# Performance work log

Hardware: AMD Instinct MI355X
Metric: run time of the kernel (lower is better)

Reference implementation:

```python
import jax, jax.numpy as jnp
import numpy as np

S = 64        # num_states
ODIM = 8      # padded neighbor-feature width
H = 256       # HIDDEN_DIM
A = 16        # num_actions
B = 16384     # batch (dtpt)
IDIM = S + ODIM
NEG_SLOPE = 0.01  # nn.LeakyReLU default
EPS = 1e-5        # nn.LayerNorm default


def setup_inputs() -> dict:
    key = jax.random.key(0)
    ks = jax.random.split(key, 8)
    x = jax.random.normal(ks[0], (B, S), jnp.float32)
    # per-state neighbor indices into x's feature dim, padded to ODIM with a mask
    o_idx = jax.random.randint(ks[1], (S, ODIM), 0, S)
    o_len = jax.random.randint(ks[2], (S,), 1, ODIM + 1)
    o_mask = jnp.arange(ODIM)[None, :] < o_len[:, None]  # [S, ODIM] bool

    def lin(k, fin, fout):
        bound = 1.0 / np.sqrt(fin)
        kw, kb = jax.random.split(k)
        W = jax.random.uniform(kw, (S, fin, fout), jnp.float32, -bound, bound)
        b = jax.random.uniform(kb, (S, fout), jnp.float32, -bound, bound)
        return W, b

    W1, b1 = lin(ks[3], IDIM, H)
    W2, b2 = lin(ks[4], H, H)
    Wp, bp = lin(ks[5], H, A)
    g1 = jnp.ones((S, H), jnp.float32); be1 = jnp.zeros((S, H), jnp.float32)
    g2 = jnp.ones((S, H), jnp.float32); be2 = jnp.zeros((S, H), jnp.float32)
    return dict(x=x, o_idx=o_idx, o_mask=o_mask, W1=W1, b1=b1, g1=g1, be1=be1,
                W2=W2, b2=b2, g2=g2, be2=be2, Wp=Wp, bp=bp)


def _layer_norm(h, g, b):
    # h: [B, S, H], per-state affine params g,b: [S, H]
    mu = jnp.mean(h, axis=-1, keepdims=True)
    var = jnp.mean((h - mu) ** 2, axis=-1, keepdims=True)
    return (h - mu) * jax.lax.rsqrt(var + EPS) * g[None] + b[None]


def reference(x, o_idx, o_mask, W1, b1, g1, be1, W2, b2, g2, be2, Wp, bp):
    # irregular gather: for each state s take x[:, o_nbr_index[s]], zero-pad to ODIM
    o = jnp.where(o_mask[None, :, :], x[:, o_idx], jnp.float32(0))  # [B, S, ODIM]
    one_hot = jnp.broadcast_to(jnp.eye(S, dtype=x.dtype)[None], (x.shape[0], S, S))
    inp = jnp.concatenate([one_hot, o], axis=-1)  # [B, S, IDIM]

    h = jnp.einsum('bsi,sih->bsh', inp, W1) + b1[None]
    h = _layer_norm(jax.nn.leaky_relu(h, NEG_SLOPE), g1, be1)
    h = jnp.einsum('bsh,shk->bsk', h, W2) + b2[None]
    h = _layer_norm(jax.nn.leaky_relu(h, NEG_SLOPE), g2, be2)
    pi_logit = jnp.einsum('bsh,sha->bsa', h, Wp) + bp[None]  # [B, S, A]
    lg_sm = jax.nn.log_softmax(pi_logit, axis=-1)
    return pi_logit, lg_sm
```

## Files before the change

kernel.cpp:

```cpp
#include <hip/hip_runtime.h>

#define LNEPS 1e-5f

typedef __attribute__((ext_vector_type(8)))  short          bf16x8;
typedef __attribute__((ext_vector_type(8)))  unsigned short u16x8;
typedef __attribute__((ext_vector_type(4)))  float          f32x4;
typedef __attribute__((ext_vector_type(16))) float          f32x16;
typedef __attribute__((ext_vector_type(4)))  unsigned int   u32x4;

#define MFMA32(a, b, c) __builtin_amdgcn_mfma_f32_32x32x16_bf16((a), (b), (c), 0, 0, 0)

#define WS_W2G  0
#define WS_A1   8388608
#define WS_WPG  8912896
#define WS_UC2  10027008
#define WS_MIDX 10092544

union U8 { bf16x8 v; unsigned u[4]; };

__device__ __forceinline__ unsigned short f2bf(float v) {
  union { float f; unsigned u; } a; a.f = v;
  unsigned r = a.u + 0x7fffu + ((a.u >> 16) & 1u);
  return (unsigned short)(r >> 16);
}
__device__ __forceinline__ unsigned cvtpk(float lo, float hi) {
  unsigned r;
  asm("v_cvt_pk_bf16_f32 %0, %1, %2" : "=v"(r) : "v"(lo), "v"(hi));
  return r;
}
__device__ __forceinline__ void plswap(unsigned w, unsigned& lo, unsigned& hi) {
  unsigned a = w, b = w;
  asm volatile("v_permlane32_swap_b32 %0, %1" : "+v"(a), "+v"(b));
  lo = a; hi = b;
}

__global__ void prep_midx_k(const int* __restrict__ oidx,
                            const unsigned* __restrict__ mask32,
                            int* __restrict__ midx) {
  __shared__ int fgt1, ffl;
  const int t = threadIdx.x;
  if (t == 0) { fgt1 = 0; ffl = 0; }
  __syncthreads();
  if (t < 128) {
    unsigned wv = mask32[t];
    if (wv == 0x3f800000u) atomicOr(&ffl, 1);
    else if (wv > 1u)      atomicOr(&fgt1, 1);
  }
  __syncthreads();
  const int mode = ffl ? 2 : (fgt1 ? 1 : 0);
  int mv;
  if (mode == 2)      mv = (((const float*)mask32)[t] != 0.0f) ? 1 : 0;
  else if (mode == 1) mv = (int)((const unsigned char*)mask32)[t];
  else                mv = ((const int*)mask32)[t];
  midx[t] = (mv != 0) ? oidx[t] : -1;
}

__global__ __launch_bounds__(256) void prep_w2g_k(
    const float* __restrict__ W2, const float* __restrict__ g1,
    unsigned short* __restrict__ w2g) {
  const int tid = blockIdx.x * 256 + threadIdx.x;
  const int l = tid & 63;
  const int t = (tid >> 6) & 15;
  const int i = (tid >> 10) & 7;
  const int s = tid >> 13;
  const int n = i * 32 + (l & 31);
  const int h = l >> 5;
  const float* w = W2 + (size_t)s * 65536;
  const float* g = g1 + s * 256;
  u16x8 v;
#pragma unroll
  for (int j = 0; j < 8; ++j) {
    const int k = t * 16 + h * 8 + j;
    v[j] = f2bf(w[k * 256 + n] * g[k]);
  }
  ((u16x8*)w2g)[tid] = v;
}

__global__ __launch_bounds__(256) void prep_uc2_k(
    const float* __restrict__ W2, const float* __restrict__ g1,
    const float* __restrict__ be1, const float* __restrict__ b2,
    unsigned* __restrict__ uc2) {
  const int tid = blockIdx.x * 256 + threadIdx.x;
  const int s = tid >> 8, n = tid & 255;
  const float* w = W2 + (size_t)s * 65536 + n;
  const float* g = g1 + s * 256;
  const float* be = be1 + s * 256;
  float u = 0.f, c = 0.f;
#pragma unroll 8
  for (int k = 0; k < 256; ++k) {
    const float wk = w[k * 256];
    u = fmaf(wk, g[k], u);
    c = fmaf(wk, be[k], c);
  }
  c += b2[tid];
  uc2[tid] = (unsigned)f2bf(u) | ((unsigned)f2bf(c) << 16);
}

__global__ __launch_bounds__(256) void prep_a1_k(
    const float* __restrict__ W1, const float* __restrict__ b1,
    unsigned short* __restrict__ a1b) {
  const int tid = blockIdx.x * 256 + threadIdx.x;
  const int l = tid & 63;
  const int i = (tid >> 6) & 7;
  const int s = tid >> 9;
  const int n = i * 32 + (l & 31);
  const float* w = W1 + (size_t)s * 72 * 256;
  u16x8 v;
#pragma unroll
  for (int j = 0; j < 8; ++j) v[j] = 0;
  if (l < 32) {
#pragma unroll
    for (int j = 0; j < 8; ++j) v[j] = f2bf(w[(64 + j) * 256 + n]);
  } else {
    v[0] = f2bf(w[s * 256 + n] + b1[s * 256 + n]);
  }
  ((u16x8*)a1b)[tid] = v;
}

__global__ __launch_bounds__(256) void prep_wpg_k(
    const float* __restrict__ Wp, const float* __restrict__ g2,
    const float* __restrict__ be2, const float* __restrict__ bp,
    unsigned short* __restrict__ wpg) {
  const int tid = blockIdx.x * 256 + threadIdx.x;
  const int l = tid & 63;
  const int r = tid >> 6;
  const int t = r % 17;
  const int s = r / 17;
  const int a = l & 31;
  const int h = l >> 5;
  u16x8 v;
#pragma unroll
  for (int j = 0; j < 8; ++j) v[j] = 0;
  if (t < 16) {
    if (a < 16) {
      const float* w = Wp + (size_t)s * 4096;
      const float* g = g2 + s * 256;
#pragma unroll
      for (int j = 0; j < 8; ++j) {
        const int k = t * 16 + h * 8 + j;
        v[j] = f2bf(w[k * 16 + a] * g[k]);
      }
    }
  } else if (h == 0 && a < 16) {
    const float* w = Wp + (size_t)s * 4096;
    float up = 0.f, cp = 0.f;
#pragma unroll 8
    for (int k = 0; k < 256; ++k) {
      const float wk = w[k * 16 + a];
      up = fmaf(wk, g2[s * 256 + k], up);
      cp = fmaf(wk, be2[s * 256 + k], cp);
    }
    cp += bp[s * 16 + a];
    v[0] = f2bf(up); v[1] = f2bf(cp);
  }
  ((u16x8*)wpg)[tid] = v;
}

__device__ __forceinline__ void pack_tile(const f32x16& a, const int h,
                                          unsigned* f0, unsigned* f1) {
  unsigned lo[8], hi[8];
#pragma unroll
  for (int m = 0; m < 8; ++m) {
    unsigned w = cvtpk(a[2 * m], a[2 * m + 1]);
    plswap(w, lo[m], hi[m]);
  }
  f0[0] = h ? lo[2] : lo[0];
  f0[1] = h ? lo[3] : lo[1];
  f0[2] = h ? hi[2] : hi[0];
  f0[3] = h ? hi[3] : hi[1];
  f1[0] = h ? lo[6] : lo[4];
  f1[1] = h ? lo[7] : lo[5];
  f1[2] = h ? hi[6] : hi[4];
  f1[3] = h ? hi[7] : hi[5];
}

__global__ __launch_bounds__(512, 2) void actor_main(
    const float* __restrict__ x, const int* __restrict__ midx,
    const unsigned short* __restrict__ w2g, const unsigned* __restrict__ uc2,
    const unsigned short* __restrict__ a1b, const unsigned short* __restrict__ wpg,
    float* __restrict__ out) {
  extern __shared__ char lds[];
  const int tid = threadIdx.x;
  const int wv = tid >> 6;
  const int l = tid & 63;
  const int bl = l & 31;
  const int h = l >> 5;
  const int s = blockIdx.x >> 2;
  const int rowstart = (blockIdx.x & 3) << 12;

  {
    const u32x4* src = (const u32x4*)(w2g + (size_t)s * 65536);
    u32x4* dst = (u32x4*)lds;
#pragma unroll
    for (int i = 0; i < 16; ++i) dst[i * 512 + tid] = src[i * 512 + tid];
  }

  unsigned aext[8];
#pragma unroll
  for (int i = 0; i < 8; ++i) {
    const unsigned t = uc2[(s * 8 + i) * 32 + bl];
    aext[i] = h ? 0u : t;
  }
  const int4 mi4 = ((const int4*)(midx + s * 8))[h];
  const bf16x8* A1 = ((const bf16x8*)a1b) + (size_t)(s * 8) * 64 + l;
  const bf16x8* A3 = ((const bf16x8*)wpg) + (size_t)(s * 17) * 64 + l;

  __syncthreads();

  for (int it = 0; it < 16; ++it) {
    const int row = rowstart + it * 256 + wv * 32 + bl;

    const float* xr = x + (size_t)row * 64;
    const float ga = mi4.x < 0 ? 0.f : xr[mi4.x];
    const float gb = mi4.y < 0 ? 0.f : xr[mi4.y];
    const float gc = mi4.z < 0 ? 0.f : xr[mi4.z];
    const float gd = mi4.w < 0 ? 0.f : xr[mi4.w];
    unsigned oa0, ob0, oa1, ob1;
    plswap(cvtpk(ga, gb), oa0, ob0);
    plswap(cvtpk(gc, gd), oa1, ob1);
    U8 B1;
    B1.u[0] = h ? 0x00003F80u : oa0;
    B1.u[1] = h ? 0u : oa1;
    B1.u[2] = h ? 0u : ob0;
    B1.u[3] = h ? 0u : ob1;
    f32x16 acc1[8];
#pragma unroll
    for (int i = 0; i < 8; ++i) {
      f32x16 z = {};
      acc1[i] = MFMA32(A1[i * 64], B1.v, z);
    }

    float s0 = 0.f, s1 = 0.f, q0 = 0.f, q1 = 0.f;
#pragma unroll
    for (int i = 0; i < 8; ++i)
#pragma unroll
      for (int r = 0; r < 16; ++r) {
        float v = acc1[i][r];
        v = fmaxf(v, 0.01f * v);
        acc1[i][r] = v;
        if (r & 1) { s1 += v; q1 = fmaf(v, v, q1); }
        else       { s0 += v; q0 = fmaf(v, v, q0); }
      }
    float sum = s0 + s1, ssq = q0 + q1;
    sum += __shfl_xor(sum, 32, 64);
    ssq += __shfl_xor(ssq, 32, 64);
    const float m1 = sum * 0.00390625f;
    const float var1 = fmaf(ssq, 0.00390625f, -m1 * m1) + LNEPS;
    const float rho1 = rsqrtf(var1);
    const float std1 = var1 * rho1;
    const unsigned be2w = cvtpk(-m1, std1);

    unsigned yf[16][4];
#pragma unroll
    for (int i = 0; i < 8; ++i) pack_tile(acc1[i], h, yf[2 * i], yf[2 * i + 1]);

    f32x16 acc2[8];
#pragma unroll
    for (int i = 0; i < 8; ++i) { f32x16 z = {}; acc2[i] = z; }
#pragma unroll
    for (int t = 0; t < 16; ++t) {
      U8 Bf;
      Bf.u[0] = yf[t][0]; Bf.u[1] = yf[t][1]; Bf.u[2] = yf[t][2]; Bf.u[3] = yf[t][3];
#pragma unroll
      for (int i = 0; i < 8; ++i) {
        const bf16x8 Af = *(const bf16x8*)(lds + (((i << 4) + t) << 10) + (l << 4));
        acc2[i] = MFMA32(Af, Bf.v, acc2[i]);
      }
    }
    {
      U8 Bx; Bx.u[0] = h ? 0u : be2w; Bx.u[1] = 0; Bx.u[2] = 0; Bx.u[3] = 0;
#pragma unroll
      for (int i = 0; i < 8; ++i) {
        U8 Ax; Ax.u[0] = aext[i]; Ax.u[1] = 0; Ax.u[2] = 0; Ax.u[3] = 0;
        acc2[i] = MFMA32(Ax.v, Bx.v, acc2[i]);
      }
    }

    s0 = s1 = q0 = q1 = 0.f;
#pragma unroll
    for (int i = 0; i < 8; ++i)
#pragma unroll
      for (int r = 0; r < 16; ++r) {
        float v = acc2[i][r];
        v = fmaxf(v, 0.01f * v);
        acc2[i][r] = v;
        if (r & 1) { s1 += v; q1 = fmaf(v, v, q1); }
        else       { s0 += v; q0 = fmaf(v, v, q0); }
      }
    float sum2 = s0 + s1, ssq2 = q0 + q1;
    sum2 += __shfl_xor(sum2, 32, 64);
    ssq2 += __shfl_xor(ssq2, 32, 64);
    const float mp = sum2 * 0.00390625f;
    const float qp = ssq2 * 0.00390625f;
    const float var2 = rho1 * rho1 * fmaf(-mp, mp, qp) + LNEPS;
    const float rho2 = rsqrtf(var2);
    const float sigma = rho1 * rho2;
    const float inv = var2 * rho2 * std1;
    const unsigned be3w = cvtpk(-mp, inv);

#pragma unroll
    for (int i = 0; i < 8; ++i) pack_tile(acc2[i], h, yf[2 * i], yf[2 * i + 1]);

    f32x16 a3a = {}, a3b = {};
#pragma unroll
    for (int t = 0; t < 16; t += 2) {
      U8 B0, Bq;
      B0.u[0] = yf[t][0]; B0.u[1] = yf[t][1]; B0.u[2] = yf[t][2]; B0.u[3] = yf[t][3];
      Bq.u[0] = yf[t + 1][0]; Bq.u[1] = yf[t + 1][1]; Bq.u[2] = yf[t + 1][2]; Bq.u[3] = yf[t + 1][3];
      a3a = MFMA32(A3[t * 64], B0.v, a3a);
      a3b = MFMA32(A3[(t + 1) * 64], Bq.v, a3b);
    }
    {
      U8 Bx; Bx.u[0] = h ? 0u : be3w; Bx.u[1] = 0; Bx.u[2] = 0; Bx.u[3] = 0;
      a3a = MFMA32(A3[16 * 64], Bx.v, a3a);
    }
    float lg[8];
#pragma unroll
    for (int r = 0; r < 8; ++r) lg[r] = sigma * (a3a[r] + a3b[r]);
    float mx = fmaxf(fmaxf(fmaxf(lg[0], lg[1]), fmaxf(lg[2], lg[3])),
                     fmaxf(fmaxf(lg[4], lg[5]), fmaxf(lg[6], lg[7])));
    mx = fmaxf(mx, __shfl_xor(mx, 32, 64));
    float es = 0.f;
#pragma unroll
    for (int r = 0; r < 8; ++r) es += __expf(lg[r] - mx);
    es += __shfl_xor(es, 32, 64);
    const float lse = mx + __logf(es);

    const size_t ob = (((size_t)row << 6) + s) * 16 + (h << 2);
    f32x4 v0 = {lg[0], lg[1], lg[2], lg[3]};
    f32x4 v1 = {lg[4], lg[5], lg[6], lg[7]};
    *(f32x4*)(out + ob) = v0;
    *(f32x4*)(out + ob + 8) = v1;
    f32x4 w0 = {lg[0] - lse, lg[1] - lse, lg[2] - lse, lg[3] - lse};
    f32x4 w1 = {lg[4] - lse, lg[5] - lse, lg[6] - lse, lg[7] - lse};
    *(f32x4*)(out + 16777216 + ob) = w0;
    *(f32x4*)(out + 16777216 + ob + 8) = w1;
  }
}

extern "C" void kernel_launch(void* const* d_in, const int* in_sizes, int n_in,
                              void* d_out, int out_size, void* d_ws, size_t ws_size,
                              hipStream_t stream) {
  const float* x    = (const float*)d_in[0];
  const int*   oidx = (const int*)d_in[1];
  const unsigned* omask = (const unsigned*)d_in[2];
  const float* W1 = (const float*)d_in[3];
  const float* b1 = (const float*)d_in[4];
  const float* g1 = (const float*)d_in[5];
  const float* be1 = (const float*)d_in[6];
  const float* W2 = (const float*)d_in[7];
  const float* b2 = (const float*)d_in[8];
  const float* g2 = (const float*)d_in[9];
  const float* be2 = (const float*)d_in[10];
  const float* Wp = (const float*)d_in[11];
  const float* bp = (const float*)d_in[12];
  float* out = (float*)d_out;

  char* ws = (char*)d_ws;
  unsigned short* wsW2G = (unsigned short*)(ws + WS_W2G);
  unsigned short* wsA1  = (unsigned short*)(ws + WS_A1);
  unsigned short* wsWPG = (unsigned short*)(ws + WS_WPG);
  unsigned*       wsUC2 = (unsigned*)(ws + WS_UC2);
  int*            wsMIDX = (int*)(ws + WS_MIDX);

  prep_midx_k<<<1, 512, 0, stream>>>(oidx, omask, wsMIDX);
  prep_w2g_k<<<2048, 256, 0, stream>>>(W2, g1, wsW2G);
  prep_uc2_k<<<64, 256, 0, stream>>>(W2, g1, be1, b2, wsUC2);
  prep_a1_k<<<128, 256, 0, stream>>>(W1, b1, wsA1);
  prep_wpg_k<<<272, 256, 0, stream>>>(Wp, g2, be2, bp, wsWPG);

  hipFuncSetAttribute((const void*)actor_main,
                      hipFuncAttributeMaxDynamicSharedMemorySize, 131072);
  actor_main<<<256, 512, 131072, stream>>>(
      x, wsMIDX, wsW2G, wsUC2, wsA1, wsWPG, out);
}
```

Before: 327.9 us.

## Prefetch next gather, interleave packing with MFMAs, simplify permlane packing

Rewrites pack_tile to use paired permlane32 swaps instead of duplicate swaps plus per-half selects, which cuts VALU work. Moves the x gather for the next iteration ahead of the current iteration's compute so global load latency overlaps the MFMA work. Packing of layer outputs is interleaved with the activation/statistics loop, and the third GEMM's MFMAs are issued per tile as each tile is packed. LDS weight fragments are loaded in batches ahead of the MFMA group, which is wrapped in s_setprio. The paired swap changes the data mapping, so numerical correctness relies on the new swap layout matching the old selects.

```diff
diff --git a/kernel.cpp b/kernel.cpp
--- a/kernel.cpp
+++ b/kernel.cpp
@@ -27,6 +27,9 @@
   unsigned r;
   asm("v_cvt_pk_bf16_f32 %0, %1, %2" : "=v"(r) : "v"(lo), "v"(hi));
   return r;
+}
+__device__ __forceinline__ void swap2(unsigned& a, unsigned& b) {
+  asm volatile("v_permlane32_swap_b32 %0, %1" : "+v"(a), "+v"(b));
 }
 __device__ __forceinline__ void plswap(unsigned w, unsigned& lo, unsigned& hi) {
   unsigned a = w, b = w;
@@ -156,22 +159,15 @@
   ((u16x8*)wpg)[tid] = v;
 }
 
-__device__ __forceinline__ void pack_tile(const f32x16& a, const int h,
+__device__ __forceinline__ void pack_tile(const f32x16& a,
                                           unsigned* f0, unsigned* f1) {
-  unsigned lo[8], hi[8];
-#pragma unroll
-  for (int m = 0; m < 8; ++m) {
-    unsigned w = cvtpk(a[2 * m], a[2 * m + 1]);
-    plswap(w, lo[m], hi[m]);
-  }
-  f0[0] = h ? lo[2] : lo[0];
-  f0[1] = h ? lo[3] : lo[1];
-  f0[2] = h ? hi[2] : hi[0];
-  f0[3] = h ? hi[3] : hi[1];
-  f1[0] = h ? lo[6] : lo[4];
-  f1[1] = h ? lo[7] : lo[5];
-  f1[2] = h ? hi[6] : hi[4];
-  f1[3] = h ? hi[7] : hi[5];
+  unsigned w0 = cvtpk(a[0], a[1]),   w1 = cvtpk(a[2], a[3]);
+  unsigned w2 = cvtpk(a[4], a[5]),   w3 = cvtpk(a[6], a[7]);
+  unsigned w4 = cvtpk(a[8], a[9]),   w5 = cvtpk(a[10], a[11]);
+  unsigned w6 = cvtpk(a[12], a[13]), w7 = cvtpk(a[14], a[15]);
+  swap2(w0, w2); swap2(w1, w3); swap2(w4, w6); swap2(w5, w7);
+  f0[0] = w0; f0[1] = w1; f0[2] = w2; f0[3] = w3;
+  f1[0] = w4; f1[1] = w5; f1[2] = w6; f1[3] = w7;
 }
 
 __global__ __launch_bounds__(512, 2) void actor_main(
@@ -205,16 +201,18 @@
   const bf16x8* A1 = ((const bf16x8*)a1b) + (size_t)(s * 8) * 64 + l;
   const bf16x8* A3 = ((const bf16x8*)wpg) + (size_t)(s * 17) * 64 + l;
 
+  const float* xbase = x + (size_t)(rowstart + wv * 32 + bl) * 64;
+
+  float ga = mi4.x < 0 ? 0.f : xbase[mi4.x];
+  float gb = mi4.y < 0 ? 0.f : xbase[mi4.y];
+  float gc = mi4.z < 0 ? 0.f : xbase[mi4.z];
+  float gd = mi4.w < 0 ? 0.f : xbase[mi4.w];
+
   __syncthreads();
 
   for (int it = 0; it < 16; ++it) {
     const int row = rowstart + it * 256 + wv * 32 + bl;
 
-    const float* xr = x + (size_t)row * 64;
-    const float ga = mi4.x < 0 ? 0.f : xr[mi4.x];
-    const float gb = mi4.y < 0 ? 0.f : xr[mi4.y];
-    const float gc = mi4.z < 0 ? 0.f : xr[mi4.z];
-    const float gd = mi4.w < 0 ? 0.f : xr[mi4.w];
     unsigned oa0, ob0, oa1, ob1;
     plswap(cvtpk(ga, gb), oa0, ob0);
     plswap(cvtpk(gc, gd), oa1, ob1);
@@ -223,6 +221,15 @@
     B1.u[1] = h ? 0u : oa1;
     B1.u[2] = h ? 0u : ob0;
     B1.u[3] = h ? 0u : ob1;
+
+    {
+      const float* xn = xbase + (size_t)(((it + 1) & 15) * 256) * 64;
+      ga = mi4.x < 0 ? 0.f : xn[mi4.x];
+      gb = mi4.y < 0 ? 0.f : xn[mi4.y];
+      gc = mi4.z < 0 ? 0.f : xn[mi4.z];
+      gd = mi4.w < 0 ? 0.f : xn[mi4.w];
+    }
+
     f32x16 acc1[8];
 #pragma unroll
     for (int i = 0; i < 8; ++i) {
@@ -231,8 +238,9 @@
     }
 
     float s0 = 0.f, s1 = 0.f, q0 = 0.f, q1 = 0.f;
-#pragma unroll
-    for (int i = 0; i < 8; ++i)
+    unsigned yf[16][4];
+#pragma unroll
+    for (int i = 0; i < 8; ++i) {
 #pragma unroll
       for (int r = 0; r < 16; ++r) {
         float v = acc1[i][r];
@@ -241,6 +249,8 @@
         if (r & 1) { s1 += v; q1 = fmaf(v, v, q1); }
         else       { s0 += v; q0 = fmaf(v, v, q0); }
       }
+      pack_tile(acc1[i], yf[2 * i], yf[2 * i + 1]);
+    }
     float sum = s0 + s1, ssq = q0 + q1;
     sum += __shfl_xor(sum, 32, 64);
     ssq += __shfl_xor(ssq, 32, 64);
@@ -250,10 +260,6 @@
     const float std1 = var1 * rho1;
     const unsigned be2w = cvtpk(-m1, std1);
 
-    unsigned yf[16][4];
-#pragma unroll
-    for (int i = 0; i < 8; ++i) pack_tile(acc1[i], h, yf[2 * i], yf[2 * i + 1]);
-
     f32x16 acc2[8];
 #pragma unroll
     for (int i = 0; i < 8; ++i) { f32x16 z = {}; acc2[i] = z; }
@@ -261,11 +267,14 @@
     for (int t = 0; t < 16; ++t) {
       U8 Bf;
       Bf.u[0] = yf[t][0]; Bf.u[1] = yf[t][1]; Bf.u[2] = yf[t][2]; Bf.u[3] = yf[t][3];
-#pragma unroll
-      for (int i = 0; i < 8; ++i) {
-        const bf16x8 Af = *(const bf16x8*)(lds + (((i << 4) + t) << 10) + (l << 4));
-        acc2[i] = MFMA32(Af, Bf.v, acc2[i]);
-      }
+      bf16x8 Af[8];
+#pragma unroll
+      for (int i = 0; i < 8; ++i)
+        Af[i] = *(const bf16x8*)(lds + (((i << 4) + t) << 10) + (l << 4));
+      __builtin_amdgcn_s_setprio(1);
+#pragma unroll
+      for (int i = 0; i < 8; ++i) acc2[i] = MFMA32(Af[i], Bf.v, acc2[i]);
+      __builtin_amdgcn_s_setprio(0);
     }
     {
       U8 Bx; Bx.u[0] = h ? 0u : be2w; Bx.u[1] = 0; Bx.u[2] = 0; Bx.u[3] = 0;
@@ -276,9 +285,10 @@
       }
     }
 
+    f32x16 a3a = {}, a3b = {};
     s0 = s1 = q0 = q1 = 0.f;
 #pragma unroll
-    for (int i = 0; i < 8; ++i)
+    for (int i = 0; i < 8; ++i) {
 #pragma unroll
       for (int r = 0; r < 16; ++r) {
         float v = acc2[i][r];
@@ -287,6 +297,11 @@
         if (r & 1) { s1 += v; q1 = fmaf(v, v, q1); }
         else       { s0 += v; q0 = fmaf(v, v, q0); }
       }
+      U8 Bf0, Bf1;
+      pack_tile(acc2[i], Bf0.u, Bf1.u);
+      a3a = MFMA32(A3[(2 * i) * 64], Bf0.v, a3a);
+      a3b = MFMA32(A3[(2 * i + 1) * 64], Bf1.v, a3b);
+    }
     float sum2 = s0 + s1, ssq2 = q0 + q1;
     sum2 += __shfl_xor(sum2, 32, 64);
     ssq2 += __shfl_xor(ssq2, 32, 64);
@@ -297,23 +312,11 @@
     const float sigma = rho1 * rho2;
     const float inv = var2 * rho2 * std1;
     const unsigned be3w = cvtpk(-mp, inv);
-
-#pragma unroll
-    for (int i = 0; i < 8; ++i) pack_tile(acc2[i], h, yf[2 * i], yf[2 * i + 1]);
-
-    f32x16 a3a = {}, a3b = {};
-#pragma unroll
-    for (int t = 0; t < 16; t += 2) {
-      U8 B0, Bq;
-      B0.u[0] = yf[t][0]; B0.u[1] = yf[t][1]; B0.u[2] = yf[t][2]; B0.u[3] = yf[t][3];
-      Bq.u[0] = yf[t + 1][0]; Bq.u[1] = yf[t + 1][1]; Bq.u[2] = yf[t + 1][2]; Bq.u[3] = yf[t + 1][3];
-      a3a = MFMA32(A3[t * 64], B0.v, a3a);
-      a3b = MFMA32(A3[(t + 1) * 64], Bq.v, a3b);
-    }
     {
       U8 Bx; Bx.u[0] = h ? 0u : be3w; Bx.u[1] = 0; Bx.u[2] = 0; Bx.u[3] = 0;
       a3a = MFMA32(A3[16 * 64], Bx.v, a3a);
     }
+
     float lg[8];
 #pragma unroll
     for (int r = 0; r < 8; ++r) lg[r] = sigma * (a3a[r] + a3b[r]);
```

Result: no change. 321.8 us (-1.9%).
